# Optimization experiments

Measured on AMD Instinct MI355X. Metric: run time of the kernel, lower is better.

The kernel has to match this reference:

```python
import jax, jax.numpy as jnp
import numpy as np

HIDDEN = 768
INTER = 2048
N_EXPERTS = 8
TOP_K = 2
SWIGLU_LIMIT = 7.0
N_TOK = 8192


def setup_inputs() -> dict:
    key = jax.random.key(0)
    k_x, k_r, k_gu, k_d = jax.random.split(key, 4)
    x = jax.random.normal(k_x, (N_TOK, HIDDEN), dtype=jnp.float32)
    router_w = jax.random.normal(k_r, (N_EXPERTS, HIDDEN), dtype=jnp.float32) * 0.02
    gate_up_proj = jax.random.normal(k_gu, (N_EXPERTS, 2 * INTER, HIDDEN), dtype=jnp.float32) * 0.02
    down_proj = jax.random.normal(k_d, (N_EXPERTS, HIDDEN, INTER), dtype=jnp.float32) * 0.02
    return {"x": x, "router_w": router_w, "gate_up_proj": gate_up_proj, "down_proj": down_proj}


def reference(x, router_w, gate_up_proj, down_proj):
    # router: [n_tok, E]
    router_logits = x @ router_w.T
    topk_vals, topk_idx = jax.lax.top_k(router_logits, TOP_K)  # [n_tok, k]
    topk_weights = jax.nn.softmax(topk_vals.astype(jnp.float32), axis=-1).astype(x.dtype)

    out = jnp.zeros_like(x)
    # Loop over the small fixed expert set; each expert is a dense GEMM over all
    # tokens, masked by its per-token routing weight (0 for unrouted tokens) —
    # identical math to the original gather/GEMM/scatter dispatch.
    for e in range(N_EXPERTS):
        # per-token weight for expert e (sums slots; each expert appears at most once per token)
        w_e = jnp.sum(jnp.where(topk_idx == e, topk_weights, 0.0), axis=-1)  # [n_tok]
        gate_up = x @ gate_up_proj[e].T  # [n_tok, 2*I]
        gate, up = jnp.split(gate_up, 2, axis=-1)
        up = jnp.minimum(up, SWIGLU_LIMIT)
        mlp_out = (jax.nn.silu(gate) * up) @ down_proj[e].T  # [n_tok, H]
        out = out + mlp_out * w_e[:, None]
    return out
```

## Files before the change

### kernel.cpp

```cpp
#include <hip/hip_runtime.h>
#include <hip/hip_bf16.h>

typedef unsigned short u16;
typedef unsigned int u32;
typedef short bf16x8 __attribute__((ext_vector_type(8)));
typedef float f32x4 __attribute__((ext_vector_type(4)));

#define NTOK 8192
#define HID 768
#define INTER 2048
#define NEXP 8

#define MFMA16(a, b, c) __builtin_amdgcn_mfma_f32_16x16x32_bf16(a, b, c, 0, 0, 0)
#define S_BARRIER() __builtin_amdgcn_s_barrier()
#define WAITVM(n) asm volatile("s_waitcnt vmcnt(" #n ")" ::: "memory")

__device__ __forceinline__ u16 f2bf(float f) {
    u32 u = __builtin_bit_cast(u32, f);
    u32 r = (u + 0x7FFFu + ((u >> 16) & 1u)) >> 16;
    return (u16)r;
}

__device__ __forceinline__ void gld16(const void* g, void* l) {
    __builtin_amdgcn_global_load_lds((const __attribute__((address_space(1))) void*)g,
                                     (__attribute__((address_space(3))) void*)l, 16, 0, 0);
}

__global__ __launch_bounds__(256) void cvt2_kernel(const float* __restrict__ s1, u16* __restrict__ d1, int n1,
                                                   const float* __restrict__ s2, u16* __restrict__ d2, int n2) {
    int i = blockIdx.x * blockDim.x + threadIdx.x;
    int stride = gridDim.x * blockDim.x;
    int ntot = n1 + n2;
    for (; i < ntot; i += stride) {
        const float* src;
        u16* dst;
        int k;
        if (i < n1) { src = s1; dst = d1; k = i; }
        else { src = s2; dst = d2; k = i - n1; }
        const float4* s = (const float4*)(src + (size_t)k * 8);
        float4 a = s[0], b = s[1];
        u16 r[8] = {f2bf(a.x), f2bf(a.y), f2bf(a.z), f2bf(a.w),
                    f2bf(b.x), f2bf(b.y), f2bf(b.z), f2bf(b.w)};
        *(uint4*)(dst + (size_t)k * 8) = *(const uint4*)r;
    }
}

__global__ __launch_bounds__(256) void router3(const float* __restrict__ x, const float* __restrict__ rw,
                                               u32* __restrict__ route, float* __restrict__ wslot,
                                               u32* __restrict__ xb32, float4* __restrict__ out4) {
    int wv = threadIdx.x >> 6, ln = threadIdx.x & 63;
    int t = blockIdx.x * 4 + wv;
    if (t >= NTOK) return;
    float4 z = {0.f, 0.f, 0.f, 0.f};
#pragma unroll
    for (int k = 0; k < 3; k++) out4[(size_t)t * 192 + ln + k * 64] = z;
    const float2* x2 = (const float2*)(x + (size_t)t * HID);
    float2 xr2[6];
#pragma unroll
    for (int j = 0; j < 6; j++) xr2[j] = x2[ln + 64 * j];
    u32* xrow = xb32 + (size_t)t * (HID / 2);
#pragma unroll
    for (int j = 0; j < 6; j++)
        xrow[ln + 64 * j] = (u32)f2bf(xr2[j].x) | ((u32)f2bf(xr2[j].y) << 16);
    float lg[NEXP];
#pragma unroll
    for (int e = 0; e < NEXP; e++) {
        const float2* rw2 = (const float2*)(rw + e * HID);
        float a = 0.f;
#pragma unroll
        for (int j = 0; j < 6; j++) {
            float2 r2 = rw2[ln + 64 * j];
            a += xr2[j].x * r2.x + xr2[j].y * r2.y;
        }
#pragma unroll
        for (int off = 32; off; off >>= 1) a += __shfl_xor(a, off);
        lg[e] = a;
    }
    int i0 = 0;
    float v0 = lg[0];
#pragma unroll
    for (int e = 1; e < NEXP; e++)
        if (lg[e] > v0) { v0 = lg[e]; i0 = e; }
    int i1 = -1;
    float v1 = -1e30f;
#pragma unroll
    for (int e = 0; e < NEXP; e++) {
        if (e == i0) continue;
        if (lg[e] > v1) { v1 = lg[e]; i1 = e; }
    }
    float w0 = 1.f / (1.f + __expf(v1 - v0));
    float w1 = 1.f - w0;
    if (ln == 0) {
        wslot[0 * NTOK + t] = w0;
        wslot[1 * NTOK + t] = w1;
        route[t] = (u32)i0 | ((u32)i1 << 8);
    }
}

__global__ __launch_bounds__(1024) void scatter_kernel(const u32* __restrict__ route, int* __restrict__ counts,
                                                       int* __restrict__ tokslot, int* __restrict__ ntiles,
                                                       int* __restrict__ tiledesc, int* __restrict__ ntiles2,
                                                       int* __restrict__ tiledesc2, int* __restrict__ ebase) {
    __shared__ int sc[NEXP][1024];
    int tid = threadIdx.x;
    u32 rt[8];
    int cnt[NEXP] = {0, 0, 0, 0, 0, 0, 0, 0};
#pragma unroll
    for (int k = 0; k < 8; k++) {
        rt[k] = route[tid * 8 + k];
        cnt[rt[k] & 255]++;
        cnt[(rt[k] >> 8) & 255]++;
    }
#pragma unroll
    for (int e = 0; e < NEXP; e++) sc[e][tid] = cnt[e];
    __syncthreads();
    for (int off = 1; off < 1024; off <<= 1) {
        int v[NEXP];
#pragma unroll
        for (int e = 0; e < NEXP; e++) v[e] = (tid >= off) ? sc[e][tid - off] : 0;
        __syncthreads();
#pragma unroll
        for (int e = 0; e < NEXP; e++)
            if (tid >= off) sc[e][tid] += v[e];
        __syncthreads();
    }
    int ebL[NEXP];
    {
        int b = 0;
#pragma unroll
        for (int e = 0; e < NEXP; e++) { ebL[e] = b; b += sc[e][1023]; }
    }
    int base[NEXP];
#pragma unroll
    for (int e = 0; e < NEXP; e++) base[e] = sc[e][tid] - cnt[e];
#pragma unroll
    for (int k = 0; k < 8; k++) {
        int t = tid * 8 + k;
        int e0 = rt[k] & 255, e1 = (rt[k] >> 8) & 255;
        tokslot[ebL[e0] + base[e0]] = t;
        base[e0]++;
        tokslot[ebL[e1] + base[e1]] = t | (1 << 16);
        base[e1]++;
    }
    if (tid == 0) {
        int tot = 0, tot2 = 0;
        for (int e = 0; e < NEXP; e++) {
            int c = sc[e][1023];
            counts[e] = c;
            ebase[e] = ebL[e];
            int nt = (c + 255) >> 8;
            for (int q = 0; q < nt; q++) tiledesc[tot++] = (e << 8) | q;
            int nt2 = (c + 191) / 192;
            for (int q = 0; q < nt2; q++) tiledesc2[tot2++] = (e << 8) | q;
        }
        ntiles[0] = tot;
        ntiles2[0] = tot2;
    }
}


#define STG(d, kt)                                           \
    do {                                                     \
        char* base_ = lds + (d)*24576 + (tid << 4);          \
        size_t ko_ = (size_t)(kt)*64;                        \
        gld16(aP[0] + ko_, base_);                           \
        gld16(aP[1] + ko_, base_ + 4096);                    \
        gld16(aP[2] + ko_, base_ + 8192);                    \
        gld16(aP[3] + ko_, base_ + 12288);                   \
        gld16(bP[0] + ko_, base_ + 16384);                   \
        gld16(bP[1] + ko_, base_ + 20480);                   \
    } while (0)

#define PIPE_MB(NKT)                                                      \
    f32x4 acc[8][4];                                                      \
    _Pragma("unroll") for (int m_ = 0; m_ < 8; m_++)                      \
        _Pragma("unroll") for (int n_ = 0; n_ < 4; n_++) acc[m_][n_] = (f32x4)0.f; \
    const int sOff = ((g4 ^ (rsel & 3) ^ ((rsel >> 2) & 3)) << 4);        \
    const int aBase = (wr * 128 + rsel) * 64 + sOff;                      \
    const int bBase = 16384 + (wc * 64 + rsel) * 64 + sOff;               \
    STG(0, 0);                                                            \
    WAITVM(0);                                                            \
    S_BARRIER();                                                          \
    for (int t = 0; t < (NKT); ++t) {                                     \
        if (t + 1 < (NKT)) STG((t + 1) & 1, t + 1);                       \
        const char* Tb = lds + (t & 1) * 24576;                           \
        bf16x8 af[8], bfr[4];                                             \
        _Pragma("unroll") for (int m_ = 0; m_ < 8; m_++)                  \
            af[m_] = *(const bf16x8*)(Tb + aBase + m_ * 1024);            \
        _Pragma("unroll") for (int n_ = 0; n_ < 4; n_++)                  \
            bfr[n_] = *(const bf16x8*)(Tb + bBase + n_ * 1024);           \
        _Pragma("unroll") for (int m_ = 0; m_ < 8; m_++)                  \
            _Pragma("unroll") for (int n_ = 0; n_ < 4; n_++)              \
                acc[m_][n_] = MFMA16(af[m_], bfr[n_], acc[m_][n_]);       \
        WAITVM(0);                                                        \
        S_BARRIER();                                                      \
    }

__global__ __launch_bounds__(256, 3) void gateup_mb(const u16* __restrict__ xb, const u16* __restrict__ gub,
                                                    const int* __restrict__ counts,
                                                    const int* __restrict__ ntiles, const int* __restrict__ tiledesc,
                                                    const int* __restrict__ tokslot, const int* __restrict__ ebase,
                                                    u16* __restrict__ h) {
    if ((int)blockIdx.y >= ntiles[0]) return;
    int td = tiledesc[blockIdx.y];
    int e = td >> 8;
    int cnt = counts[e];
    int eb = ebase[e];
    int row0 = (td & 255) * 256;
    int c0 = blockIdx.x * 64;

    extern __shared__ char lds[];
    int tid = threadIdx.x;
    int wv = tid >> 6, ln = tid & 63;
    int wr = wv >> 1, wc = wv & 1;
    int rsel = ln & 15, g4 = ln >> 4;

    int srow = tid >> 2, sl = tid & 3;
    int sswz = ((sl ^ (srow & 3) ^ ((srow >> 2) & 3)) << 4);
    const char* aP[4];
    const char* bP[2];
#pragma unroll
    for (int c = 0; c < 4; c++) {
        int gr = row0 + c * 64 + srow;
        gr = gr < cnt ? gr : cnt - 1;
        int tok = tokslot[eb + gr] & 0xFFFF;
        aP[c] = (const char*)xb + (size_t)tok * (HID * 2) + sswz;
    }
#pragma unroll
    for (int c = 0; c < 2; c++) {
        int r = c * 64 + srow;
        int wi = r & 63;
        int b = (wi >> 5) * 2048 + c0 + (r >> 6) * 32 + (wi & 31);
        bP[c] = (const char*)gub + ((size_t)e * 4096 + b) * (HID * 2) + sswz;
    }

    PIPE_MB(HID / 32)

#pragma unroll
    for (int mg = 0; mg < 8; mg++) {
#pragma unroll
        for (int j = 0; j < 4; j++) {
            int gr = row0 + wr * 128 + mg * 16 + g4 * 4 + j;
            if (gr >= cnt) continue;
            u16* hrow = h + (size_t)(eb + gr) * INTER;
#pragma unroll
            for (int n = 0; n < 2; n++) {
                float gv = acc[mg][n][j];
                float uv = fminf(acc[mg][n + 2][j], 7.0f);
                float sg = gv / (1.0f + __expf(-gv));
                hrow[c0 + wc * 32 + n * 16 + rsel] = f2bf(sg * uv);
            }
        }
    }
}

#define DSTG(d, kt)                                          \
    do {                                                     \
        char* base_ = lds + (d)*20480 + (tid << 4);          \
        size_t ko_ = (size_t)(kt)*64;                        \
        gld16(aP[0] + ko_, base_);                           \
        gld16(aP[1] + ko_, base_ + 4096);                    \
        gld16(aP[2] + ko_, base_ + 8192);                    \
        gld16(bP[0] + ko_, base_ + 12288);                   \
        gld16(bP[1] + ko_, base_ + 16384);                   \
    } while (0)

__global__ __launch_bounds__(256, 3) void down_mb(const u16* __restrict__ hb, const u16* __restrict__ dnb,
                                                  const int* __restrict__ counts,
                                                  const int* __restrict__ ntiles2, const int* __restrict__ tiledesc2,
                                                  const int* __restrict__ tokslot, const int* __restrict__ ebase,
                                                  const float* __restrict__ wslot, float* __restrict__ out) {
    if ((int)blockIdx.y >= ntiles2[0]) return;
    int td = tiledesc2[blockIdx.y];
    int e = td >> 8;
    int cnt = counts[e];
    int eb = ebase[e];
    int row0 = (td & 255) * 192;
    int col0 = blockIdx.x * 128;

    extern __shared__ char lds[];
    int tid = threadIdx.x;
    int wv = tid >> 6, ln = tid & 63;
    int wr = wv >> 1, wc = wv & 1;
    int rsel = ln & 15, g4 = ln >> 4;

    int srow = tid >> 2, sl = tid & 3;
    int sswz = ((sl ^ (srow & 3) ^ ((srow >> 2) & 3)) << 4);
    const char* aP[3];
    const char* bP[2];
#pragma unroll
    for (int c = 0; c < 3; c++) {
        int gr = row0 + c * 64 + srow;
        gr = gr < cnt ? gr : cnt - 1;
        aP[c] = (const char*)hb + (size_t)(eb + gr) * (INTER * 2) + sswz;
    }
#pragma unroll
    for (int c = 0; c < 2; c++) {
        int r = c * 64 + srow;
        bP[c] = (const char*)dnb + ((size_t)e * HID + col0 + r) * (INTER * 2) + sswz;
    }

    f32x4 acc[6][4];
#pragma unroll
    for (int m_ = 0; m_ < 6; m_++)
#pragma unroll
        for (int n_ = 0; n_ < 4; n_++) acc[m_][n_] = (f32x4)0.f;
    const int sOff = ((g4 ^ (rsel & 3) ^ ((rsel >> 2) & 3)) << 4);
    const int aBase = (wr * 96 + rsel) * 64 + sOff;
    const int bBase = 12288 + (wc * 64 + rsel) * 64 + sOff;
    DSTG(0, 0);
    WAITVM(0);
    S_BARRIER();
    const int NKT = INTER / 32;
    for (int t = 0; t < NKT; ++t) {
        if (t + 1 < NKT) DSTG((t + 1) & 1, t + 1);
        const char* Tb = lds + (t & 1) * 20480;
        bf16x8 af[6], bfr[4];
#pragma unroll
        for (int m_ = 0; m_ < 6; m_++)
            af[m_] = *(const bf16x8*)(Tb + aBase + m_ * 1024);
#pragma unroll
        for (int n_ = 0; n_ < 4; n_++)
            bfr[n_] = *(const bf16x8*)(Tb + bBase + n_ * 1024);
#pragma unroll
        for (int m_ = 0; m_ < 6; m_++)
#pragma unroll
            for (int n_ = 0; n_ < 4; n_++)
                acc[m_][n_] = MFMA16(af[m_], bfr[n_], acc[m_][n_]);
        WAITVM(0);
        S_BARRIER();
    }

#pragma unroll
    for (int mg = 0; mg < 6; mg++) {
#pragma unroll
        for (int j = 0; j < 4; j++) {
            int gr = row0 + wr * 96 + mg * 16 + g4 * 4 + j;
            if (gr >= cnt) continue;
            int ts = tokslot[eb + gr];
            int tok = ts & 0xFFFF, slot = ts >> 16;
            float w = wslot[slot * NTOK + tok];
#pragma unroll
            for (int n = 0; n < 4; n++) {
                int col = col0 + wc * 64 + n * 16 + rsel;
                atomicAdd(&out[(size_t)tok * HID + col], w * acc[mg][n][j]);
            }
        }
    }
}

extern "C" void kernel_launch(void* const* d_in, const int* in_sizes, int n_in,
                              void* d_out, int out_size, void* d_ws, size_t ws_size,
                              hipStream_t stream) {
    const float* x = (const float*)d_in[0];
    const float* rw = (const float*)d_in[1];
    const float* gu = (const float*)d_in[2];
    const float* dn = (const float*)d_in[3];
    float* out = (float*)d_out;
    char* ws = (char*)d_ws;

    int* counts = (int*)(ws + 0);
    int* ntiles = (int*)(ws + 64);
    int* ntiles2 = (int*)(ws + 96);
    int* ebase = (int*)(ws + 128);
    int* tiledesc = (int*)(ws + 256);
    int* tiledesc2 = (int*)(ws + 1024);
    int* tokslot = (int*)(ws + 4096);
    float* wslot = (float*)(ws + 69632);
    u16* xb = (u16*)(ws + 135168);
    u16* gub = (u16*)(ws + 12718080);
    u16* dnb = (u16*)(ws + 63049728);
    u16* hb = (u16*)(ws + 88215552);
    u32* route = (u32*)(ws + 88215552);

    cvt2_kernel<<<2048, 256, 0, stream>>>(gu, gub, NEXP * 2 * INTER * HID / 8,
                                          dn, dnb, NEXP * HID * INTER / 8);
    router3<<<NTOK / 4, 256, 0, stream>>>(x, rw, route, wslot, (u32*)xb, (float4*)out);
    scatter_kernel<<<1, 1024, 0, stream>>>(route, counts, tokslot, ntiles, tiledesc, ntiles2, tiledesc2, ebase);
    gateup_mb<<<dim3(32, 72), 256, 49152, stream>>>(xb, gub, counts, ntiles, tiledesc, tokslot, ebase, hb);
    down_mb<<<dim3(6, 96), 256, 40960, stream>>>(hb, dnb, counts, ntiles2, tiledesc2, tokslot, ebase, wslot, out);
}
```

Before: 331.7 us.

## Enlarge MoE GEMM tiles and fuse weight conversion with routing scatter

```diff
diff --git a/kernel.cpp b/kernel.cpp
--- a/kernel.cpp
+++ b/kernel.cpp
@@ -24,25 +24,6 @@
 __device__ __forceinline__ void gld16(const void* g, void* l) {
     __builtin_amdgcn_global_load_lds((const __attribute__((address_space(1))) void*)g,
                                      (__attribute__((address_space(3))) void*)l, 16, 0, 0);
-}
-
-__global__ __launch_bounds__(256) void cvt2_kernel(const float* __restrict__ s1, u16* __restrict__ d1, int n1,
-                                                   const float* __restrict__ s2, u16* __restrict__ d2, int n2) {
-    int i = blockIdx.x * blockDim.x + threadIdx.x;
-    int stride = gridDim.x * blockDim.x;
-    int ntot = n1 + n2;
-    for (; i < ntot; i += stride) {
-        const float* src;
-        u16* dst;
-        int k;
-        if (i < n1) { src = s1; dst = d1; k = i; }
-        else { src = s2; dst = d2; k = i - n1; }
-        const float4* s = (const float4*)(src + (size_t)k * 8);
-        float4 a = s[0], b = s[1];
-        u16 r[8] = {f2bf(a.x), f2bf(a.y), f2bf(a.z), f2bf(a.w),
-                    f2bf(b.x), f2bf(b.y), f2bf(b.z), f2bf(b.w)};
-        *(uint4*)(dst + (size_t)k * 8) = *(const uint4*)r;
-    }
 }
 
 __global__ __launch_bounds__(256) void router3(const float* __restrict__ x, const float* __restrict__ rw,
@@ -97,69 +78,183 @@
     }
 }
 
-__global__ __launch_bounds__(1024) void scatter_kernel(const u32* __restrict__ route, int* __restrict__ counts,
-                                                       int* __restrict__ tokslot, int* __restrict__ ntiles,
-                                                       int* __restrict__ tiledesc, int* __restrict__ ntiles2,
-                                                       int* __restrict__ tiledesc2, int* __restrict__ ebase) {
-    __shared__ int sc[NEXP][1024];
+__global__ __launch_bounds__(1024) void prep_kernel(const u32* __restrict__ route, int* __restrict__ counts,
+                                                    int* __restrict__ tokslot, int* __restrict__ ntiles,
+                                                    int* __restrict__ tiledesc, int* __restrict__ ebase,
+                                                    const float* __restrict__ s1, u16* __restrict__ d1, int n1,
+                                                    const float* __restrict__ s2, u16* __restrict__ d2, int n2) {
     int tid = threadIdx.x;
-    u32 rt[8];
-    int cnt[NEXP] = {0, 0, 0, 0, 0, 0, 0, 0};
-#pragma unroll
-    for (int k = 0; k < 8; k++) {
-        rt[k] = route[tid * 8 + k];
-        cnt[rt[k] & 255]++;
-        cnt[(rt[k] >> 8) & 255]++;
-    }
-#pragma unroll
-    for (int e = 0; e < NEXP; e++) sc[e][tid] = cnt[e];
-    __syncthreads();
-    for (int off = 1; off < 1024; off <<= 1) {
-        int v[NEXP];
-#pragma unroll
-        for (int e = 0; e < NEXP; e++) v[e] = (tid >= off) ? sc[e][tid - off] : 0;
+    if (blockIdx.x == 0) {
+        __shared__ int sc[NEXP][1024];
+        u32 rt[8];
+        int cnt[NEXP] = {0, 0, 0, 0, 0, 0, 0, 0};
+#pragma unroll
+        for (int k = 0; k < 8; k++) {
+            rt[k] = route[tid * 8 + k];
+            cnt[rt[k] & 255]++;
+            cnt[(rt[k] >> 8) & 255]++;
+        }
+#pragma unroll
+        for (int e = 0; e < NEXP; e++) sc[e][tid] = cnt[e];
         __syncthreads();
-#pragma unroll
-        for (int e = 0; e < NEXP; e++)
-            if (tid >= off) sc[e][tid] += v[e];
-        __syncthreads();
-    }
-    int ebL[NEXP];
-    {
-        int b = 0;
-#pragma unroll
-        for (int e = 0; e < NEXP; e++) { ebL[e] = b; b += sc[e][1023]; }
-    }
-    int base[NEXP];
-#pragma unroll
-    for (int e = 0; e < NEXP; e++) base[e] = sc[e][tid] - cnt[e];
-#pragma unroll
-    for (int k = 0; k < 8; k++) {
-        int t = tid * 8 + k;
-        int e0 = rt[k] & 255, e1 = (rt[k] >> 8) & 255;
-        tokslot[ebL[e0] + base[e0]] = t;
-        base[e0]++;
-        tokslot[ebL[e1] + base[e1]] = t | (1 << 16);
-        base[e1]++;
-    }
-    if (tid == 0) {
-        int tot = 0, tot2 = 0;
-        for (int e = 0; e < NEXP; e++) {
-            int c = sc[e][1023];
-            counts[e] = c;
-            ebase[e] = ebL[e];
-            int nt = (c + 255) >> 8;
-            for (int q = 0; q < nt; q++) tiledesc[tot++] = (e << 8) | q;
-            int nt2 = (c + 191) / 192;
-            for (int q = 0; q < nt2; q++) tiledesc2[tot2++] = (e << 8) | q;
-        }
-        ntiles[0] = tot;
-        ntiles2[0] = tot2;
-    }
-}
-
-
-#define STG(d, kt)                                           \
+        for (int off = 1; off < 1024; off <<= 1) {
+            int v[NEXP];
+#pragma unroll
+            for (int e = 0; e < NEXP; e++) v[e] = (tid >= off) ? sc[e][tid - off] : 0;
+            __syncthreads();
+#pragma unroll
+            for (int e = 0; e < NEXP; e++)
+                if (tid >= off) sc[e][tid] += v[e];
+            __syncthreads();
+        }
+        int ebL[NEXP];
+        {
+            int b = 0;
+#pragma unroll
+            for (int e = 0; e < NEXP; e++) { ebL[e] = b; b += sc[e][1023]; }
+        }
+        int base[NEXP];
+#pragma unroll
+        for (int e = 0; e < NEXP; e++) base[e] = sc[e][tid] - cnt[e];
+#pragma unroll
+        for (int k = 0; k < 8; k++) {
+            int t = tid * 8 + k;
+            int e0 = rt[k] & 255, e1 = (rt[k] >> 8) & 255;
+            tokslot[ebL[e0] + base[e0]] = t;
+            base[e0]++;
+            tokslot[ebL[e1] + base[e1]] = t | (1 << 16);
+            base[e1]++;
+        }
+        if (tid == 0) {
+            int tot = 0;
+            for (int e = 0; e < NEXP; e++) {
+                int c = sc[e][1023];
+                counts[e] = c;
+                ebase[e] = ebL[e];
+                int nt = (c + 255) >> 8;
+                for (int q = 0; q < nt; q++) tiledesc[tot++] = (e << 8) | q;
+            }
+            ntiles[0] = tot;
+        }
+    } else {
+        int i = (blockIdx.x - 1) * 1024 + tid;
+        int stride = (gridDim.x - 1) * 1024;
+        int ntot = n1 + n2;
+        for (; i < ntot; i += stride) {
+            const float* src;
+            u16* dst;
+            int k;
+            if (i < n1) { src = s1; dst = d1; k = i; }
+            else { src = s2; dst = d2; k = i - n1; }
+            const float4* s = (const float4*)(src + (size_t)k * 8);
+            float4 a = s[0], b = s[1];
+            u16 r[8] = {f2bf(a.x), f2bf(a.y), f2bf(a.z), f2bf(a.w),
+                        f2bf(b.x), f2bf(b.y), f2bf(b.z), f2bf(b.w)};
+            *(uint4*)(dst + (size_t)k * 8) = *(const uint4*)r;
+        }
+    }
+}
+
+
+#define GSTG(d, kt)                                          \
+    do {                                                     \
+        char* base_ = lds + (d)*32768 + (tid << 4);          \
+        size_t ko_ = (size_t)(kt)*64;                        \
+        gld16(aP[0] + ko_, base_);                           \
+        gld16(aP[1] + ko_, base_ + 8192);                    \
+        gld16(bP[0] + ko_, base_ + 16384);                   \
+        gld16(bP[1] + ko_, base_ + 24576);                   \
+    } while (0)
+
+__global__ __launch_bounds__(512, 4) void gateup_mb8(const u16* __restrict__ xb, const u16* __restrict__ gub,
+                                                     const int* __restrict__ counts,
+                                                     const int* __restrict__ ntiles, const int* __restrict__ tiledesc,
+                                                     const int* __restrict__ tokslot, const int* __restrict__ ebase,
+                                                     u16* __restrict__ h) {
+    if ((int)blockIdx.y >= ntiles[0]) return;
+    int td = tiledesc[blockIdx.y];
+    int e = td >> 8;
+    int cnt = counts[e];
+    int eb = ebase[e];
+    int row0 = (td & 255) * 256;
+    int c0 = blockIdx.x * 128;
+
+    extern __shared__ char lds[];
+    int tid = threadIdx.x;
+    int wv = tid >> 6, ln = tid & 63;
+    int wr = wv >> 2, wc = wv & 3;
+    int rsel = ln & 15, g4 = ln >> 4;
+
+    int srow = tid >> 2, sl = tid & 3;
+    int sswz = ((sl ^ (srow & 3) ^ ((srow >> 2) & 3)) << 4);
+    const char* aP[2];
+    const char* bP[2];
+#pragma unroll
+    for (int c = 0; c < 2; c++) {
+        int gr = row0 + c * 128 + srow;
+        gr = gr < cnt ? gr : cnt - 1;
+        int tok = tokslot[eb + gr] & 0xFFFF;
+        aP[c] = (const char*)xb + (size_t)tok * (HID * 2) + sswz;
+    }
+#pragma unroll
+    for (int c = 0; c < 2; c++) {
+        int r = c * 128 + srow;
+        int wi = r & 63;
+        int b = (wi >> 5) * 2048 + c0 + (r >> 6) * 32 + (wi & 31);
+        bP[c] = (const char*)gub + ((size_t)e * 4096 + b) * (HID * 2) + sswz;
+    }
+
+    f32x4 acc[8][4];
+#pragma unroll
+    for (int m_ = 0; m_ < 8; m_++)
+#pragma unroll
+        for (int n_ = 0; n_ < 4; n_++) acc[m_][n_] = (f32x4)0.f;
+    const int sOff = ((g4 ^ (rsel & 3) ^ ((rsel >> 2) & 3)) << 4);
+    const int aBase = (wr * 128 + rsel) * 64 + sOff;
+    const int bBase = 16384 + (wc * 64 + rsel) * 64 + sOff;
+    GSTG(0, 0);
+    WAITVM(0);
+    S_BARRIER();
+    const int NKT = HID / 32;
+    for (int t = 0; t < NKT; ++t) {
+        if (t + 1 < NKT) GSTG((t + 1) & 1, t + 1);
+        const char* Tb = lds + (t & 1) * 32768;
+        bf16x8 af[8], bfr[4];
+#pragma unroll
+        for (int m_ = 0; m_ < 8; m_++)
+            af[m_] = *(const bf16x8*)(Tb + aBase + m_ * 1024);
+#pragma unroll
+        for (int n_ = 0; n_ < 4; n_++)
+            bfr[n_] = *(const bf16x8*)(Tb + bBase + n_ * 1024);
+#pragma unroll
+        for (int m_ = 0; m_ < 8; m_++)
+#pragma unroll
+            for (int n_ = 0; n_ < 4; n_++)
+                acc[m_][n_] = MFMA16(af[m_], bfr[n_], acc[m_][n_]);
+        WAITVM(0);
+        S_BARRIER();
+    }
+
+#pragma unroll
+    for (int mg = 0; mg < 8; mg++) {
+#pragma unroll
+        for (int j = 0; j < 4; j++) {
+            int gr = row0 + wr * 128 + mg * 16 + g4 * 4 + j;
+            if (gr >= cnt) continue;
+            u16* hrow = h + (size_t)(eb + gr) * INTER;
+#pragma unroll
+            for (int n = 0; n < 2; n++) {
+                float gv = acc[mg][n][j];
+                float uv = fminf(acc[mg][n + 2][j], 7.0f);
+                float sg = gv / (1.0f + __expf(-gv));
+                hrow[c0 + wc * 32 + n * 16 + rsel] = f2bf(sg * uv);
+            }
+        }
+    }
+}
+
+
+#define DSTG(d, kt)                                          \
     do {                                                     \
         char* base_ = lds + (d)*24576 + (tid << 4);          \
         size_t ko_ = (size_t)(kt)*64;                        \
@@ -171,43 +266,18 @@
         gld16(bP[1] + ko_, base_ + 20480);                   \
     } while (0)
 
-#define PIPE_MB(NKT)                                                      \
-    f32x4 acc[8][4];                                                      \
-    _Pragma("unroll") for (int m_ = 0; m_ < 8; m_++)                      \
-        _Pragma("unroll") for (int n_ = 0; n_ < 4; n_++) acc[m_][n_] = (f32x4)0.f; \
-    const int sOff = ((g4 ^ (rsel & 3) ^ ((rsel >> 2) & 3)) << 4);        \
-    const int aBase = (wr * 128 + rsel) * 64 + sOff;                      \
-    const int bBase = 16384 + (wc * 64 + rsel) * 64 + sOff;               \
-    STG(0, 0);                                                            \
-    WAITVM(0);                                                            \
-    S_BARRIER();                                                          \
-    for (int t = 0; t < (NKT); ++t) {                                     \
-        if (t + 1 < (NKT)) STG((t + 1) & 1, t + 1);                       \
-        const char* Tb = lds + (t & 1) * 24576;                           \
-        bf16x8 af[8], bfr[4];                                             \
-        _Pragma("unroll") for (int m_ = 0; m_ < 8; m_++)                  \
-            af[m_] = *(const bf16x8*)(Tb + aBase + m_ * 1024);            \
-        _Pragma("unroll") for (int n_ = 0; n_ < 4; n_++)                  \
-            bfr[n_] = *(const bf16x8*)(Tb + bBase + n_ * 1024);           \
-        _Pragma("unroll") for (int m_ = 0; m_ < 8; m_++)                  \
-            _Pragma("unroll") for (int n_ = 0; n_ < 4; n_++)              \
-                acc[m_][n_] = MFMA16(af[m_], bfr[n_], acc[m_][n_]);       \
-        WAITVM(0);                                                        \
-        S_BARRIER();                                                      \
-    }
-
-__global__ __launch_bounds__(256, 3) void gateup_mb(const u16* __restrict__ xb, const u16* __restrict__ gub,
-                                                    const int* __restrict__ counts,
-                                                    const int* __restrict__ ntiles, const int* __restrict__ tiledesc,
-                                                    const int* __restrict__ tokslot, const int* __restrict__ ebase,
-                                                    u16* __restrict__ h) {
+__global__ __launch_bounds__(256, 3) void down_mb(const u16* __restrict__ hb, const u16* __restrict__ dnb,
+                                                  const int* __restrict__ counts,
+                                                  const int* __restrict__ ntiles, const int* __restrict__ tiledesc,
+                                                  const int* __restrict__ tokslot, const int* __restrict__ ebase,
+                                                  const float* __restrict__ wslot, float* __restrict__ out) {
     if ((int)blockIdx.y >= ntiles[0]) return;
     int td = tiledesc[blockIdx.y];
     int e = td >> 8;
     int cnt = counts[e];
     int eb = ebase[e];
     int row0 = (td & 255) * 256;
-    int c0 = blockIdx.x * 64;
+    int col0 = blockIdx.x * 128;
 
     extern __shared__ char lds[];
     int tid = threadIdx.x;
@@ -223,75 +293,6 @@
     for (int c = 0; c < 4; c++) {
         int gr = row0 + c * 64 + srow;
         gr = gr < cnt ? gr : cnt - 1;
-        int tok = tokslot[eb + gr] & 0xFFFF;
-        aP[c] = (const char*)xb + (size_t)tok * (HID * 2) + sswz;
-    }
-#pragma unroll
-    for (int c = 0; c < 2; c++) {
-        int r = c * 64 + srow;
-        int wi = r & 63;
-        int b = (wi >> 5) * 2048 + c0 + (r >> 6) * 32 + (wi & 31);
-        bP[c] = (const char*)gub + ((size_t)e * 4096 + b) * (HID * 2) + sswz;
-    }
-
-    PIPE_MB(HID / 32)
-
-#pragma unroll
-    for (int mg = 0; mg < 8; mg++) {
-#pragma unroll
-        for (int j = 0; j < 4; j++) {
-            int gr = row0 + wr * 128 + mg * 16 + g4 * 4 + j;
-            if (gr >= cnt) continue;
-            u16* hrow = h + (size_t)(eb + gr) * INTER;
-#pragma unroll
-            for (int n = 0; n < 2; n++) {
-                float gv = acc[mg][n][j];
-                float uv = fminf(acc[mg][n + 2][j], 7.0f);
-                float sg = gv / (1.0f + __expf(-gv));
-                hrow[c0 + wc * 32 + n * 16 + rsel] = f2bf(sg * uv);
-            }
-        }
-    }
-}
-
-#define DSTG(d, kt)                                          \
-    do {                                                     \
-        char* base_ = lds + (d)*20480 + (tid << 4);          \
-        size_t ko_ = (size_t)(kt)*64;                        \
-        gld16(aP[0] + ko_, base_);                           \
-        gld16(aP[1] + ko_, base_ + 4096);                    \
-        gld16(aP[2] + ko_, base_ + 8192);                    \
-        gld16(bP[0] + ko_, base_ + 12288);                   \
-        gld16(bP[1] + ko_, base_ + 16384);                   \
-    } while (0)
-
-__global__ __launch_bounds__(256, 3) void down_mb(const u16* __restrict__ hb, const u16* __restrict__ dnb,
-                                                  const int* __restrict__ counts,
-                                                  const int* __restrict__ ntiles2, const int* __restrict__ tiledesc2,
-                                                  const int* __restrict__ tokslot, const int* __restrict__ ebase,
-                                                  const float* __restrict__ wslot, float* __restrict__ out) {
-    if ((int)blockIdx.y >= ntiles2[0]) return;
-    int td = tiledesc2[blockIdx.y];
-    int e = td >> 8;
-    int cnt = counts[e];
-    int eb = ebase[e];
-    int row0 = (td & 255) * 192;
-    int col0 = blockIdx.x * 128;
-
-    extern __shared__ char lds[];
-    int tid = threadIdx.x;
-    int wv = tid >> 6, ln = tid & 63;
-    int wr = wv >> 1, wc = wv & 1;
-    int rsel = ln & 15, g4 = ln >> 4;
-
-    int srow = tid >> 2, sl = tid & 3;
-    int sswz = ((sl ^ (srow & 3) ^ ((srow >> 2) & 3)) << 4);
-    const char* aP[3];
-    const char* bP[2];
-#pragma unroll
-    for (int c = 0; c < 3; c++) {
-        int gr = row0 + c * 64 + srow;
-        gr = gr < cnt ? gr : cnt - 1;
         aP[c] = (const char*)hb + (size_t)(eb + gr) * (INTER * 2) + sswz;
     }
 #pragma unroll
@@ -300,30 +301,30 @@
         bP[c] = (const char*)dnb + ((size_t)e * HID + col0 + r) * (INTER * 2) + sswz;
     }
 
-    f32x4 acc[6][4];
-#pragma unroll
-    for (int m_ = 0; m_ < 6; m_++)
+    f32x4 acc[8][4];
+#pragma unroll
+    for (int m_ = 0; m_ < 8; m_++)
 #pragma unroll
         for (int n_ = 0; n_ < 4; n_++) acc[m_][n_] = (f32x4)0.f;
     const int sOff = ((g4 ^ (rsel & 3) ^ ((rsel >> 2) & 3)) << 4);
-    const int aBase = (wr * 96 + rsel) * 64 + sOff;
-    const int bBase = 12288 + (wc * 64 + rsel) * 64 + sOff;
+    const int aBase = (wr * 128 + rsel) * 64 + sOff;
+    const int bBase = 16384 + (wc * 64 + rsel) * 64 + sOff;
     DSTG(0, 0);
     WAITVM(0);
     S_BARRIER();
     const int NKT = INTER / 32;
     for (int t = 0; t < NKT; ++t) {
         if (t + 1 < NKT) DSTG((t + 1) & 1, t + 1);
-        const char* Tb = lds + (t & 1) * 20480;
-        bf16x8 af[6], bfr[4];
-#pragma unroll
-        for (int m_ = 0; m_ < 6; m_++)
+        const char* Tb = lds + (t & 1) * 24576;
+        bf16x8 af[8], bfr[4];
+#pragma unroll
+        for (int m_ = 0; m_ < 8; m_++)
             af[m_] = *(const bf16x8*)(Tb + aBase + m_ * 1024);
 #pragma unroll
         for (int n_ = 0; n_ < 4; n_++)
             bfr[n_] = *(const bf16x8*)(Tb + bBase + n_ * 1024);
 #pragma unroll
-        for (int m_ = 0; m_ < 6; m_++)
+        for (int m_ = 0; m_ < 8; m_++)
 #pragma unroll
             for (int n_ = 0; n_ < 4; n_++)
                 acc[m_][n_] = MFMA16(af[m_], bfr[n_], acc[m_][n_]);
@@ -332,10 +333,10 @@
     }
 
 #pragma unroll
-    for (int mg = 0; mg < 6; mg++) {
+    for (int mg = 0; mg < 8; mg++) {
 #pragma unroll
         for (int j = 0; j < 4; j++) {
-            int gr = row0 + wr * 96 + mg * 16 + g4 * 4 + j;
+            int gr = row0 + wr * 128 + mg * 16 + g4 * 4 + j;
             if (gr >= cnt) continue;
             int ts = tokslot[eb + gr];
             int tok = ts & 0xFFFF, slot = ts >> 16;
@@ -361,10 +362,8 @@
 
     int* counts = (int*)(ws + 0);
     int* ntiles = (int*)(ws + 64);
-    int* ntiles2 = (int*)(ws + 96);
     int* ebase = (int*)(ws + 128);
     int* tiledesc = (int*)(ws + 256);
-    int* tiledesc2 = (int*)(ws + 1024);
     int* tokslot = (int*)(ws + 4096);
     float* wslot = (float*)(ws + 69632);
     u16* xb = (u16*)(ws + 135168);
@@ -373,10 +372,10 @@
     u16* hb = (u16*)(ws + 88215552);
     u32* route = (u32*)(ws + 88215552);
 
-    cvt2_kernel<<<2048, 256, 0, stream>>>(gu, gub, NEXP * 2 * INTER * HID / 8,
-                                          dn, dnb, NEXP * HID * INTER / 8);
     router3<<<NTOK / 4, 256, 0, stream>>>(x, rw, route, wslot, (u32*)xb, (float4*)out);
-    scatter_kernel<<<1, 1024, 0, stream>>>(route, counts, tokslot, ntiles, tiledesc, ntiles2, tiledesc2, ebase);
-    gateup_mb<<<dim3(32, 72), 256, 49152, stream>>>(xb, gub, counts, ntiles, tiledesc, tokslot, ebase, hb);
-    down_mb<<<dim3(6, 96), 256, 40960, stream>>>(hb, dnb, counts, ntiles2, tiledesc2, tokslot, ebase, wslot, out);
-}
+    prep_kernel<<<2048, 1024, 0, stream>>>(route, counts, tokslot, ntiles, tiledesc, ebase,
+                                           gu, gub, NEXP * 2 * INTER * HID / 8,
+                                           dn, dnb, NEXP * HID * INTER / 8);
+    gateup_mb8<<<dim3(16, 72), 512, 65536, stream>>>(xb, gub, counts, ntiles, tiledesc, tokslot, ebase, hb);
+    down_mb<<<dim3(6, 72), 256, 49152, stream>>>(hb, dnb, counts, ntiles, tiledesc, tokslot, ebase, wslot, out);
+}
```

Measured after the change: 895.4 us. 170% more time.

## Fuse weight conversion with scatter and use 256-row tiles in down GEMM

Applied to the files above, without the earlier changes.

```diff
diff --git a/kernel.cpp b/kernel.cpp
--- a/kernel.cpp
+++ b/kernel.cpp
@@ -24,25 +24,6 @@
 __device__ __forceinline__ void gld16(const void* g, void* l) {
     __builtin_amdgcn_global_load_lds((const __attribute__((address_space(1))) void*)g,
                                      (__attribute__((address_space(3))) void*)l, 16, 0, 0);
-}
-
-__global__ __launch_bounds__(256) void cvt2_kernel(const float* __restrict__ s1, u16* __restrict__ d1, int n1,
-                                                   const float* __restrict__ s2, u16* __restrict__ d2, int n2) {
-    int i = blockIdx.x * blockDim.x + threadIdx.x;
-    int stride = gridDim.x * blockDim.x;
-    int ntot = n1 + n2;
-    for (; i < ntot; i += stride) {
-        const float* src;
-        u16* dst;
-        int k;
-        if (i < n1) { src = s1; dst = d1; k = i; }
-        else { src = s2; dst = d2; k = i - n1; }
-        const float4* s = (const float4*)(src + (size_t)k * 8);
-        float4 a = s[0], b = s[1];
-        u16 r[8] = {f2bf(a.x), f2bf(a.y), f2bf(a.z), f2bf(a.w),
-                    f2bf(b.x), f2bf(b.y), f2bf(b.z), f2bf(b.w)};
-        *(uint4*)(dst + (size_t)k * 8) = *(const uint4*)r;
-    }
 }
 
 __global__ __launch_bounds__(256) void router3(const float* __restrict__ x, const float* __restrict__ rw,
@@ -97,64 +78,80 @@
     }
 }
 
-__global__ __launch_bounds__(1024) void scatter_kernel(const u32* __restrict__ route, int* __restrict__ counts,
-                                                       int* __restrict__ tokslot, int* __restrict__ ntiles,
-                                                       int* __restrict__ tiledesc, int* __restrict__ ntiles2,
-                                                       int* __restrict__ tiledesc2, int* __restrict__ ebase) {
-    __shared__ int sc[NEXP][1024];
+__global__ __launch_bounds__(1024) void prep_kernel(const u32* __restrict__ route, int* __restrict__ counts,
+                                                    int* __restrict__ tokslot, int* __restrict__ ntiles,
+                                                    int* __restrict__ tiledesc, int* __restrict__ ebase,
+                                                    const float* __restrict__ s1, u16* __restrict__ d1, int n1,
+                                                    const float* __restrict__ s2, u16* __restrict__ d2, int n2) {
     int tid = threadIdx.x;
-    u32 rt[8];
-    int cnt[NEXP] = {0, 0, 0, 0, 0, 0, 0, 0};
-#pragma unroll
-    for (int k = 0; k < 8; k++) {
-        rt[k] = route[tid * 8 + k];
-        cnt[rt[k] & 255]++;
-        cnt[(rt[k] >> 8) & 255]++;
-    }
-#pragma unroll
-    for (int e = 0; e < NEXP; e++) sc[e][tid] = cnt[e];
-    __syncthreads();
-    for (int off = 1; off < 1024; off <<= 1) {
-        int v[NEXP];
-#pragma unroll
-        for (int e = 0; e < NEXP; e++) v[e] = (tid >= off) ? sc[e][tid - off] : 0;
+    if (blockIdx.x == 0) {
+        __shared__ int sc[NEXP][1024];
+        u32 rt[8];
+        int cnt[NEXP] = {0, 0, 0, 0, 0, 0, 0, 0};
+#pragma unroll
+        for (int k = 0; k < 8; k++) {
+            rt[k] = route[tid * 8 + k];
+            cnt[rt[k] & 255]++;
+            cnt[(rt[k] >> 8) & 255]++;
+        }
+#pragma unroll
+        for (int e = 0; e < NEXP; e++) sc[e][tid] = cnt[e];
         __syncthreads();
-#pragma unroll
-        for (int e = 0; e < NEXP; e++)
-            if (tid >= off) sc[e][tid] += v[e];
-        __syncthreads();
-    }
-    int ebL[NEXP];
-    {
-        int b = 0;
-#pragma unroll
-        for (int e = 0; e < NEXP; e++) { ebL[e] = b; b += sc[e][1023]; }
-    }
-    int base[NEXP];
-#pragma unroll
-    for (int e = 0; e < NEXP; e++) base[e] = sc[e][tid] - cnt[e];
-#pragma unroll
-    for (int k = 0; k < 8; k++) {
-        int t = tid * 8 + k;
-        int e0 = rt[k] & 255, e1 = (rt[k] >> 8) & 255;
-        tokslot[ebL[e0] + base[e0]] = t;
-        base[e0]++;
-        tokslot[ebL[e1] + base[e1]] = t | (1 << 16);
-        base[e1]++;
-    }
-    if (tid == 0) {
-        int tot = 0, tot2 = 0;
-        for (int e = 0; e < NEXP; e++) {
-            int c = sc[e][1023];
-            counts[e] = c;
-            ebase[e] = ebL[e];
-            int nt = (c + 255) >> 8;
-            for (int q = 0; q < nt; q++) tiledesc[tot++] = (e << 8) | q;
-            int nt2 = (c + 191) / 192;
-            for (int q = 0; q < nt2; q++) tiledesc2[tot2++] = (e << 8) | q;
-        }
-        ntiles[0] = tot;
-        ntiles2[0] = tot2;
+        for (int off = 1; off < 1024; off <<= 1) {
+            int v[NEXP];
+#pragma unroll
+            for (int e = 0; e < NEXP; e++) v[e] = (tid >= off) ? sc[e][tid - off] : 0;
+            __syncthreads();
+#pragma unroll
+            for (int e = 0; e < NEXP; e++)
+                if (tid >= off) sc[e][tid] += v[e];
+            __syncthreads();
+        }
+        int ebL[NEXP];
+        {
+            int b = 0;
+#pragma unroll
+            for (int e = 0; e < NEXP; e++) { ebL[e] = b; b += sc[e][1023]; }
+        }
+        int base[NEXP];
+#pragma unroll
+        for (int e = 0; e < NEXP; e++) base[e] = sc[e][tid] - cnt[e];
+#pragma unroll
+        for (int k = 0; k < 8; k++) {
+            int t = tid * 8 + k;
+            int e0 = rt[k] & 255, e1 = (rt[k] >> 8) & 255;
+            tokslot[ebL[e0] + base[e0]] = t;
+            base[e0]++;
+            tokslot[ebL[e1] + base[e1]] = t | (1 << 16);
+            base[e1]++;
+        }
+        if (tid == 0) {
+            int tot = 0;
+            for (int e = 0; e < NEXP; e++) {
+                int c = sc[e][1023];
+                counts[e] = c;
+                ebase[e] = ebL[e];
+                int nt = (c + 255) >> 8;
+                for (int q = 0; q < nt; q++) tiledesc[tot++] = (e << 8) | q;
+            }
+            ntiles[0] = tot;
+        }
+    } else {
+        int i = (blockIdx.x - 1) * 1024 + tid;
+        int stride = (gridDim.x - 1) * 1024;
+        int ntot = n1 + n2;
+        for (; i < ntot; i += stride) {
+            const float* src;
+            u16* dst;
+            int k;
+            if (i < n1) { src = s1; dst = d1; k = i; }
+            else { src = s2; dst = d2; k = i - n1; }
+            const float4* s = (const float4*)(src + (size_t)k * 8);
+            float4 a = s[0], b = s[1];
+            u16 r[8] = {f2bf(a.x), f2bf(a.y), f2bf(a.z), f2bf(a.w),
+                        f2bf(b.x), f2bf(b.y), f2bf(b.z), f2bf(b.w)};
+            *(uint4*)(dst + (size_t)k * 8) = *(const uint4*)r;
+        }
     }
 }
 
@@ -254,28 +251,18 @@
     }
 }
 
-#define DSTG(d, kt)                                          \
-    do {                                                     \
-        char* base_ = lds + (d)*20480 + (tid << 4);          \
-        size_t ko_ = (size_t)(kt)*64;                        \
-        gld16(aP[0] + ko_, base_);                           \
-        gld16(aP[1] + ko_, base_ + 4096);                    \
-        gld16(aP[2] + ko_, base_ + 8192);                    \
-        gld16(bP[0] + ko_, base_ + 12288);                   \
-        gld16(bP[1] + ko_, base_ + 16384);                   \
-    } while (0)
 
 __global__ __launch_bounds__(256, 3) void down_mb(const u16* __restrict__ hb, const u16* __restrict__ dnb,
                                                   const int* __restrict__ counts,
-                                                  const int* __restrict__ ntiles2, const int* __restrict__ tiledesc2,
+                                                  const int* __restrict__ ntiles, const int* __restrict__ tiledesc,
                                                   const int* __restrict__ tokslot, const int* __restrict__ ebase,
                                                   const float* __restrict__ wslot, float* __restrict__ out) {
-    if ((int)blockIdx.y >= ntiles2[0]) return;
-    int td = tiledesc2[blockIdx.y];
+    if ((int)blockIdx.y >= ntiles[0]) return;
+    int td = tiledesc[blockIdx.y];
     int e = td >> 8;
     int cnt = counts[e];
     int eb = ebase[e];
-    int row0 = (td & 255) * 192;
+    int row0 = (td & 255) * 256;
     int col0 = blockIdx.x * 128;
 
     extern __shared__ char lds[];
@@ -286,10 +273,10 @@
 
     int srow = tid >> 2, sl = tid & 3;
     int sswz = ((sl ^ (srow & 3) ^ ((srow >> 2) & 3)) << 4);
-    const char* aP[3];
+    const char* aP[4];
     const char* bP[2];
 #pragma unroll
-    for (int c = 0; c < 3; c++) {
+    for (int c = 0; c < 4; c++) {
         int gr = row0 + c * 64 + srow;
         gr = gr < cnt ? gr : cnt - 1;
         aP[c] = (const char*)hb + (size_t)(eb + gr) * (INTER * 2) + sswz;
@@ -300,42 +287,13 @@
         bP[c] = (const char*)dnb + ((size_t)e * HID + col0 + r) * (INTER * 2) + sswz;
     }
 
-    f32x4 acc[6][4];
-#pragma unroll
-    for (int m_ = 0; m_ < 6; m_++)
-#pragma unroll
-        for (int n_ = 0; n_ < 4; n_++) acc[m_][n_] = (f32x4)0.f;
-    const int sOff = ((g4 ^ (rsel & 3) ^ ((rsel >> 2) & 3)) << 4);
-    const int aBase = (wr * 96 + rsel) * 64 + sOff;
-    const int bBase = 12288 + (wc * 64 + rsel) * 64 + sOff;
-    DSTG(0, 0);
-    WAITVM(0);
-    S_BARRIER();
-    const int NKT = INTER / 32;
-    for (int t = 0; t < NKT; ++t) {
-        if (t + 1 < NKT) DSTG((t + 1) & 1, t + 1);
-        const char* Tb = lds + (t & 1) * 20480;
-        bf16x8 af[6], bfr[4];
-#pragma unroll
-        for (int m_ = 0; m_ < 6; m_++)
-            af[m_] = *(const bf16x8*)(Tb + aBase + m_ * 1024);
-#pragma unroll
-        for (int n_ = 0; n_ < 4; n_++)
-            bfr[n_] = *(const bf16x8*)(Tb + bBase + n_ * 1024);
-#pragma unroll
-        for (int m_ = 0; m_ < 6; m_++)
-#pragma unroll
-            for (int n_ = 0; n_ < 4; n_++)
-                acc[m_][n_] = MFMA16(af[m_], bfr[n_], acc[m_][n_]);
-        WAITVM(0);
-        S_BARRIER();
-    }
-
-#pragma unroll
-    for (int mg = 0; mg < 6; mg++) {
+    PIPE_MB(INTER / 32)
+
+#pragma unroll
+    for (int mg = 0; mg < 8; mg++) {
 #pragma unroll
         for (int j = 0; j < 4; j++) {
-            int gr = row0 + wr * 96 + mg * 16 + g4 * 4 + j;
+            int gr = row0 + wr * 128 + mg * 16 + g4 * 4 + j;
             if (gr >= cnt) continue;
             int ts = tokslot[eb + gr];
             int tok = ts & 0xFFFF, slot = ts >> 16;
@@ -361,10 +319,8 @@
 
     int* counts = (int*)(ws + 0);
     int* ntiles = (int*)(ws + 64);
-    int* ntiles2 = (int*)(ws + 96);
     int* ebase = (int*)(ws + 128);
     int* tiledesc = (int*)(ws + 256);
-    int* tiledesc2 = (int*)(ws + 1024);
     int* tokslot = (int*)(ws + 4096);
     float* wslot = (float*)(ws + 69632);
     u16* xb = (u16*)(ws + 135168);
@@ -373,10 +329,10 @@
     u16* hb = (u16*)(ws + 88215552);
     u32* route = (u32*)(ws + 88215552);
 
-    cvt2_kernel<<<2048, 256, 0, stream>>>(gu, gub, NEXP * 2 * INTER * HID / 8,
-                                          dn, dnb, NEXP * HID * INTER / 8);
     router3<<<NTOK / 4, 256, 0, stream>>>(x, rw, route, wslot, (u32*)xb, (float4*)out);
-    scatter_kernel<<<1, 1024, 0, stream>>>(route, counts, tokslot, ntiles, tiledesc, ntiles2, tiledesc2, ebase);
+    prep_kernel<<<2048, 1024, 0, stream>>>(route, counts, tokslot, ntiles, tiledesc, ebase,
+                                           gu, gub, NEXP * 2 * INTER * HID / 8,
+                                           dn, dnb, NEXP * HID * INTER / 8);
     gateup_mb<<<dim3(32, 72), 256, 49152, stream>>>(xb, gub, counts, ntiles, tiledesc, tokslot, ebase, hb);
-    down_mb<<<dim3(6, 96), 256, 40960, stream>>>(hb, dnb, counts, ntiles2, tiledesc2, tokslot, ebase, wslot, out);
-}
+    down_mb<<<dim3(6, 72), 256, 49152, stream>>>(hb, dnb, counts, ntiles, tiledesc, tokslot, ebase, wslot, out);
+}
```

Result: faster. 302.5 us (median of 2 runs) (-8.8%).
